# Optimization experiments

Hardware: AMD Instinct MI355X
Metric: run time of the kernel (lower is better)

Reference implementation:

```python
import jax, jax.numpy as jnp
import numpy as np

S, D = 16384, 1024


def setup_inputs() -> dict:
    key = jax.random.key(0)
    ks = jax.random.split(key, 7)
    stdv = 1.0 / np.sqrt(D)
    u = lambda k, shape: jax.random.uniform(k, shape, jnp.float32, -stdv, stdv)
    return {
        "x": jax.random.normal(ks[0], (S, D), jnp.float32),
        "Wq": u(ks[1], (D, D)), "bq": u(ks[2], (D,)),
        "Wk": u(ks[3], (D, D)), "bk": u(ks[4], (D,)),
        "Wv": u(ks[5], (D, D)), "bv": u(ks[6], (D,)),
    }


def reference(x, Wq, bq, Wk, bk, Wv, bv):
    # torch.nn.Linear: y = x @ W^T + b
    q = x @ Wq.T + bq          # [S, D]
    k = x @ Wk.T + bk          # [S, D]
    v = x @ Wv.T + bv          # [S, D]
    d = x.shape[-1]
    # NOTE: faithful to source -- scores are over the FEATURE axis: [D, D]
    scores = jnp.einsum('sd,se->de', q, k) / jnp.sqrt(jnp.float32(d))
    attn = jax.nn.softmax(scores, axis=-1)   # [D, D]
    out = v @ attn                           # [S, D]
    return out, attn
```

## Files before the change

kernel.cpp:

```cpp
#include <hip/hip_runtime.h>
#include <hip/hip_bf16.h>
#include <stdint.h>


#define S_ 16384
#define D_ 1024

typedef _Float16 half8 __attribute__((ext_vector_type(8)));
typedef _Float16 half4 __attribute__((ext_vector_type(4)));
typedef float f32x4 __attribute__((ext_vector_type(4)));

__device__ __forceinline__ void gload_lds16(const _Float16* g, _Float16* l) {
    __builtin_amdgcn_global_load_lds(
        (const __attribute__((address_space(1))) void*)g,
        (__attribute__((address_space(3))) void*)l, 16, 0, 0);
}

#define VM8() do { asm volatile("s_waitcnt vmcnt(8)" ::: "memory"); __builtin_amdgcn_sched_barrier(0); } while (0)
#define VM0() do { asm volatile("s_waitcnt vmcnt(0)" ::: "memory"); __builtin_amdgcn_sched_barrier(0); } while (0)
#define BAR() __builtin_amdgcn_s_barrier()
#define LGKM0() do { asm volatile("s_waitcnt lgkmcnt(0)" ::: "memory"); __builtin_amdgcn_sched_barrier(0); } while (0)
#define LGKM8() do { asm volatile("s_waitcnt lgkmcnt(8)" ::: "memory"); __builtin_amdgcn_sched_barrier(0); } while (0)
#define PRIO1() __builtin_amdgcn_s_setprio(1)
#define PRIO0() __builtin_amdgcn_s_setprio(0)

#define STAGEA(H, KT, NX) do { \
    const _Float16* _s = srcA + (size_t)((H) * 128) * lda + (size_t)(KT) * 64; \
    _Float16* _d = AsS + (NX) * 16384 + ((H) * 128 + 8 * w) * 64; \
    gload_lds16(_s, _d); \
    gload_lds16(_s + (size_t)64 * lda, _d + 4096); \
} while (0)

#define STAGEB(H, KT, NX) do { \
    const _Float16* _s = srcB + (size_t)((H) * 128) * ldb + (size_t)(KT) * 64; \
    _Float16* _d = BsS + (NX) * 16384 + ((H) * 128 + 8 * w) * 64; \
    gload_lds16(_s, _d); \
    gload_lds16(_s + (size_t)64 * ldb, _d + 4096); \
} while (0)

#define READA(PA, QA) do { _Pragma("unroll") \
    for (int fm = 0; fm < 4; ++fm) { \
        af[fm][0] = *(const half8*)((PA) + (((QA) * 128 + fm * 16) << 7) + cx0); \
        af[fm][1] = *(const half8*)((PA) + (((QA) * 128 + fm * 16) << 7) + cx1); } \
} while (0)

#define READB(PB, BF, QB) do { _Pragma("unroll") \
    for (int fn = 0; fn < 2; ++fn) { \
        BF[fn][0] = *(const half8*)((PB) + (((QB) * 128 + fn * 16) << 7) + cx0); \
        BF[fn][1] = *(const half8*)((PB) + (((QB) * 128 + fn * 16) << 7) + cx1); } \
} while (0)

#define MFMAB(QA, QB, BF) do { _Pragma("unroll") \
    for (int fm = 0; fm < 4; ++fm) { _Pragma("unroll") \
        for (int fn = 0; fn < 2; ++fn) { \
            f32x4 _c = acc[(QA) * 4 + fm][(QB) * 2 + fn]; \
            _c = __builtin_amdgcn_mfma_f32_16x16x32_f16(af[fm][0], BF[fn][0], _c, 0, 0, 0); \
            _c = __builtin_amdgcn_mfma_f32_16x16x32_f16(af[fm][1], BF[fn][1], _c, 0, 0, 0); \
            acc[(QA) * 4 + fm][(QB) * 2 + fn] = _c; } } \
} while (0)

__global__ __launch_bounds__(512, 2)
void gemm256(const _Float16* __restrict__ A, const _Float16* __restrict__ B,
             _Float16* __restrict__ C,
             int lda, int ldb, int ldc, int ksub, long long mn,
             int ntx, int ntxy, int cpx) {
    __shared__ _Float16 As[2][16384];
    __shared__ _Float16 Bs[2][16384];
    const int t = threadIdx.x;
    const int l = t & 63;
    const int w = t >> 6;
    const int wm = w >> 2, wn = w & 3;

    const int hb = blockIdx.x;
    const int lg = (hb & 7) * cpx + (hb >> 3);
    const int bz = lg / ntxy;
    const int rem = lg - bz * ntxy;
    const int by = rem / ntx;
    const int bx = rem - by * ntx;
    const size_t m0 = (size_t)by * 256;
    const size_t n0 = (size_t)bx * 256;
    const size_t k0 = (size_t)bz * (size_t)ksub;
    const long long coff = (long long)bz * mn;

    const int colsw = 8 * ((l & 7) ^ (l >> 3));
    const _Float16* srcA = A + (m0 + 8 * w + (l >> 3)) * (size_t)lda + k0 + colsw;
    const _Float16* srcB = B + (n0 + 8 * w + (l >> 3)) * (size_t)ldb + k0 + colsw;
    _Float16* AsS = &As[0][0];
    _Float16* BsS = &Bs[0][0];

    const int cx0 = (((l >> 4) << 4)) ^ ((l & 7) << 4);
    const int cx1 = (64 + ((l >> 4) << 4)) ^ ((l & 7) << 4);
    const char* basePA = (const char*)AsS + ((wm * 64 + (l & 15)) << 7);
    const char* basePB = (const char*)BsS + ((wn * 32 + (l & 15)) << 7);

    f32x4 acc[8][4] = {};
    half8 af[4][2], bf0[2][2], bf1[2][2];

    const int nk = ksub >> 6;

    STAGEA(0, 0, 0); STAGEB(0, 0, 0); STAGEB(1, 0, 0); STAGEA(1, 0, 0);
    STAGEA(0, 1, 1); STAGEB(0, 1, 1); STAGEB(1, 1, 1); STAGEA(1, 1, 1);

    for (int kt = 0; kt < nk; ++kt) {
        const int p = kt & 1;
        const int ks = kt + 2;
        const bool hs = ks < nk;
        const char* pA = basePA + p * 32768;
        const char* pB = basePB + p * 32768;

        if (kt == nk - 1) VM0(); else VM8();
        BAR();

        READA(pA, 0); READB(pB, bf0, 0);
        LGKM8();
        BAR(); LGKM0();
        PRIO1(); MFMAB(0, 0, bf0); PRIO0(); BAR();

        READB(pB, bf1, 1);
        if (hs) { STAGEA(0, ks, p); STAGEB(0, ks, p); }
        BAR(); LGKM0();
        PRIO1(); MFMAB(0, 1, bf1); PRIO0(); BAR();

        READA(pA, 1);
        if (hs) STAGEB(1, ks, p);
        BAR(); LGKM0();
        PRIO1(); MFMAB(1, 1, bf1); PRIO0(); BAR();

        if (hs) STAGEA(1, ks, p);
        PRIO1(); MFMAB(1, 0, bf0); PRIO0(); BAR();
    }

    char* lmy = (char*)AsS + w * 16384;
    const int cr = (l >> 4) << 2;
    const int cc = l & 15;
    _Float16* lw = (_Float16*)lmy;
#pragma unroll
    for (int h = 0; h < 2; ++h) {
#pragma unroll
        for (int mm = 0; mm < 4; ++mm) {
#pragma unroll
            for (int n = 0; n < 4; ++n) {
                const int lcol = (n >> 1) * 32 + (n & 1) * 16 + cc;
                const int lrow = mm * 16 + cr;
#pragma unroll
                for (int r = 0; r < 4; ++r)
                    lw[(lrow + r) * 68 + lcol] = (_Float16)acc[4 * h + mm][n][r];
            }
        }
        LGKM0();
        const size_t grow0 = m0 + (size_t)h * 128 + wm * 64;
#pragma unroll
        for (int i = 0; i < 32; ++i) {
            const int lrow = i * 2 + (l >> 5);
            const int lcol2 = (l & 31) * 2;
            const uint32_t v = *(const uint32_t*)(lw + lrow * 68 + lcol2);
            const int qb = lcol2 >> 5;
            const size_t col = n0 + qb * 128 + wn * 32 + (lcol2 & 31);
            __builtin_nontemporal_store(v,
                (uint32_t*)(C + coff + (long long)(grow0 + lrow) * ldc + col));
        }
        LGKM0();
    }
}

#define STG128(SRC, LD, DST, KT) do { \
    const _Float16* _s = (SRC) + (size_t)(KT) * 64; \
    _Float16* _d = (DST) + 8 * w * 64; \
    gload_lds16(_s, _d); \
    gload_lds16(_s + (size_t)32 * (LD), _d + 2048); \
    gload_lds16(_s + (size_t)64 * (LD), _d + 4096); \
    gload_lds16(_s + (size_t)96 * (LD), _d + 6144); \
} while (0)

__global__ __launch_bounds__(256, 2)
void gemm128(const _Float16* __restrict__ A, const _Float16* __restrict__ B,
             float* __restrict__ C, const float* __restrict__ bias,
             int lda, int ldb, int ldc, int ksub,
             int ntx, int cpx) {
    __shared__ _Float16 SM[32768];
    const int t = threadIdx.x;
    const int l = t & 63;
    const int w = t >> 6;
    const int wm = w >> 1, wn = w & 1;

    const int hb = blockIdx.x;
    const int lg = (hb & 7) * cpx + (hb >> 3);
    const int by = lg / ntx;
    const int bx = lg - by * ntx;
    const size_t m0 = (size_t)by * 128;
    const size_t n0 = (size_t)bx * 128;

    const int colsw = 8 * ((l & 7) ^ (l >> 3));
    const _Float16* srcA = A + (m0 + 8 * w + (l >> 3)) * (size_t)lda + colsw;
    const _Float16* srcB = B + (n0 + 8 * w + (l >> 3)) * (size_t)ldb + colsw;

    const int cx0 = (((l >> 4) << 4)) ^ ((l & 7) << 4);
    const int cx1 = (64 + ((l >> 4) << 4)) ^ ((l & 7) << 4);
    const char* basePA = (const char*)SM + ((wm * 64 + (l & 15)) << 7);
    const char* basePB = (const char*)SM + 32768 + ((wn * 64 + (l & 15)) << 7);

    f32x4 acc[4][4] = {};
    half8 af[4][2], bf[4][2];

    const int nk = ksub >> 6;

    STG128(srcA, lda, SM + 0, 0);        STG128(srcB, ldb, SM + 16384, 0);
    STG128(srcA, lda, SM + 8192, 1);     STG128(srcB, ldb, SM + 24576, 1);

    for (int kt = 0; kt < nk; ++kt) {
        const int p = kt & 1;
        const int ks = kt + 2;
        const bool hs = ks < nk;
        const char* pA = basePA + p * 16384;
        const char* pB = basePB + p * 16384;

        if (kt == nk - 1) VM0(); else VM8();
        BAR();

#pragma unroll
        for (int fm = 0; fm < 4; ++fm) {
            af[fm][0] = *(const half8*)(pA + ((fm * 16) << 7) + cx0);
            af[fm][1] = *(const half8*)(pA + ((fm * 16) << 7) + cx1);
        }
#pragma unroll
        for (int fn = 0; fn < 4; ++fn) {
            bf[fn][0] = *(const half8*)(pB + ((fn * 16) << 7) + cx0);
            bf[fn][1] = *(const half8*)(pB + ((fn * 16) << 7) + cx1);
        }
        LGKM0();
        PRIO1();
#pragma unroll
        for (int fm = 0; fm < 4; ++fm)
#pragma unroll
            for (int fn = 0; fn < 4; ++fn)
                acc[fm][fn] = __builtin_amdgcn_mfma_f32_16x16x32_f16(af[fm][0], bf[fn][0], acc[fm][fn], 0, 0, 0);
        PRIO0();
        BAR();

        if (hs) {
            STG128(srcA, lda, SM + p * 8192, ks);
            STG128(srcB, ldb, SM + 16384 + p * 8192, ks);
        }
        PRIO1();
#pragma unroll
        for (int fm = 0; fm < 4; ++fm)
#pragma unroll
            for (int fn = 0; fn < 4; ++fn)
                acc[fm][fn] = __builtin_amdgcn_mfma_f32_16x16x32_f16(af[fm][1], bf[fn][1], acc[fm][fn], 0, 0, 0);
        PRIO0();
        BAR();
    }

    float* lw = (float*)((char*)SM + w * 16384);
    const int cr = (l >> 4) << 2;
    const int cc = l & 15;
    float bb4[4];
#pragma unroll
    for (int fn = 0; fn < 4; ++fn)
        bb4[fn] = bias[n0 + wn * 64 + fn * 16 + cc];
#pragma unroll
    for (int h = 0; h < 2; ++h) {
#pragma unroll
        for (int mm2 = 0; mm2 < 2; ++mm2) {
            const int mm = h * 2 + mm2;
#pragma unroll
            for (int fn = 0; fn < 4; ++fn) {
                const int lcol = fn * 16 + cc;
                const int lrow = mm2 * 16 + cr;
#pragma unroll
                for (int r = 0; r < 4; ++r)
                    lw[(lrow + r) * 68 + lcol] = acc[mm][fn][r] + bb4[fn];
            }
        }
        LGKM0();
        const size_t grow0 = m0 + (size_t)wm * 64 + h * 32;
#pragma unroll
        for (int i = 0; i < 8; ++i) {
            const int lrow = i * 4 + (l >> 4);
            const int lcol = (l & 15) * 4;
            const f32x4 v = *(const f32x4*)(lw + lrow * 68 + lcol);
            __builtin_nontemporal_store(v,
                (f32x4*)(C + (size_t)(grow0 + lrow) * ldc + n0 + wn * 64 + lcol));
        }
        LGKM0();
    }
}

__global__ __launch_bounds__(256, 2)
void gemm_abt(const _Float16* __restrict__ A, const _Float16* __restrict__ B,
              float* __restrict__ C, int lda, int ldb, int ldc, int ksub,
              long long mn) {
    const int t = threadIdx.x;
    const int lane = t & 63;
    const int wave = t >> 6;
    const int wr = (wave >> 1) * 64;
    const int wc = (wave & 1) * 64;
    const size_t m0 = (size_t)blockIdx.y * 128;
    const size_t n0 = (size_t)blockIdx.x * 128;
    const size_t k0 = (size_t)blockIdx.z * (size_t)ksub;
    const long long coff = (long long)blockIdx.z * mn;

    __shared__ _Float16 As[128 * 32];
    __shared__ _Float16 Bs[128 * 32];

    f32x4 acc[4][4] = {};

    const _Float16* a0 = A + (m0 + (size_t)(t >> 2)) * (size_t)lda + k0 + (t & 3) * 8;
    const _Float16* a1 = a0 + (size_t)64 * lda;
    const _Float16* b0 = B + (n0 + (size_t)(t >> 2)) * (size_t)ldb + k0 + (t & 3) * 8;
    const _Float16* b1 = b0 + (size_t)64 * ldb;
    _Float16* AsW0 = As + wave * 512;
    _Float16* AsW1 = As + 2048 + wave * 512;
    _Float16* BsW0 = Bs + wave * 512;
    _Float16* BsW1 = Bs + 2048 + wave * 512;

    const int nk = ksub >> 5;
    for (int kt = 0; kt < nk; ++kt) {
        __syncthreads();
        gload_lds16(a0, AsW0);
        gload_lds16(a1, AsW1);
        gload_lds16(b0, BsW0);
        gload_lds16(b1, BsW1);
        a0 += 32; a1 += 32; b0 += 32; b1 += 32;
        __syncthreads();

        half8 af[4], bf[4];
#pragma unroll
        for (int i = 0; i < 4; ++i)
            af[i] = *(const half8*)(As + (wr + i * 16 + (lane & 15)) * 32 + (lane >> 4) * 8);
#pragma unroll
        for (int i = 0; i < 4; ++i)
            bf[i] = *(const half8*)(Bs + (wc + i * 16 + (lane & 15)) * 32 + (lane >> 4) * 8);
#pragma unroll
        for (int i = 0; i < 4; ++i)
#pragma unroll
            for (int j = 0; j < 4; ++j)
                acc[i][j] = __builtin_amdgcn_mfma_f32_16x16x32_f16(af[i], bf[j], acc[i][j], 0, 0, 0);
    }

    const int cr = (lane >> 4) * 4;
    const int cc = lane & 15;
#pragma unroll
    for (int i = 0; i < 4; ++i) {
#pragma unroll
        for (int j = 0; j < 4; ++j) {
            const size_t row0 = m0 + wr + i * 16 + cr;
            const size_t col = n0 + wc + j * 16 + cc;
#pragma unroll
            for (int r = 0; r < 4; ++r)
                C[coff + (long long)(row0 + r) * ldc + col] = acc[i][j][r];
        }
    }
}

template <int WRITE_ROW, int COLSUM>
__global__ __launch_bounds__(256)
void cast_transpose(const float* __restrict__ in, _Float16* __restrict__ outRow,
                    _Float16* __restrict__ outT, float* __restrict__ msum, int ldT) {
    __shared__ _Float16 tile[64][66];
    __shared__ float red[16][16][4];
    const int t = threadIdx.x;
    const int c0 = blockIdx.x * 64;
    const int r0 = blockIdx.y * 64;
    const int cg = t & 15;
    const int rb = t >> 4;
    f32x4 csum = {};
#pragma unroll
    for (int it = 0; it < 4; ++it) {
        const int rr = rb + it * 16;
        f32x4 v = *(const f32x4*)(in + (size_t)(r0 + rr) * 1024 + c0 + cg * 4);
        if (COLSUM) { csum[0] += v[0]; csum[1] += v[1]; csum[2] += v[2]; csum[3] += v[3]; }
        _Float16 h0 = (_Float16)v[0], h1 = (_Float16)v[1];
        _Float16 h2 = (_Float16)v[2], h3 = (_Float16)v[3];
        tile[rr][cg * 4 + 0] = h0; tile[rr][cg * 4 + 1] = h1;
        tile[rr][cg * 4 + 2] = h2; tile[rr][cg * 4 + 3] = h3;
        if (WRITE_ROW) {
            half4 h = {h0, h1, h2, h3};
            *(half4*)(outRow + (size_t)(r0 + rr) * 1024 + c0 + cg * 4) = h;
        }
    }
    if (COLSUM) {
        red[rb][cg][0] = csum[0]; red[rb][cg][1] = csum[1];
        red[rb][cg][2] = csum[2]; red[rb][cg][3] = csum[3];
    }
    __syncthreads();
    if (COLSUM && t < 64) {
        float s = 0.f;
#pragma unroll
        for (int k = 0; k < 16; ++k) s += red[k][t >> 2][t & 3];
        atomicAdd(msum + c0 + t, s);
    }
    const int i = t >> 2, ch = (t & 3) * 16;
    half8 h0v, h1v;
#pragma unroll
    for (int j = 0; j < 8; ++j) h0v[j] = tile[ch + j][i];
#pragma unroll
    for (int j = 0; j < 8; ++j) h1v[j] = tile[ch + 8 + j][i];
    *(half8*)(outT + (size_t)(c0 + i) * ldT + r0 + ch) = h0v;
    *(half8*)(outT + (size_t)(c0 + i) * ldT + r0 + ch + 8) = h1v;
}

__global__ __launch_bounds__(256)
void prep_w(const float* __restrict__ Wq, const float* __restrict__ Wk,
            const float* __restrict__ Wv, const float* __restrict__ bq,
            const float* __restrict__ m,
            _Float16* __restrict__ wq16, _Float16* __restrict__ wk16,
            _Float16* __restrict__ wvT16,
            float* __restrict__ u2, float* __restrict__ w) {
    __shared__ _Float16 tile[64][66];
    __shared__ float wred[4];
    const int b = blockIdx.x;
    const int t = threadIdx.x;

    if (b < 1024) {
        const bool isQ = b < 512;
        const int bb = isQ ? b : b - 512;
        const float* W = isQ ? Wq : Wk;
        _Float16* o = isQ ? wq16 : wk16;
        const size_t base = (size_t)bb * 2048 + (size_t)t * 8;
        const f32x4* p = (const f32x4*)(W + base);
        f32x4 x0 = p[0], x1 = p[1];
        half8 h;
        h[0] = (_Float16)x0[0]; h[1] = (_Float16)x0[1];
        h[2] = (_Float16)x0[2]; h[3] = (_Float16)x0[3];
        h[4] = (_Float16)x1[0]; h[5] = (_Float16)x1[1];
        h[6] = (_Float16)x1[2]; h[7] = (_Float16)x1[3];
        ((half8*)o)[bb * 256 + t] = h;
        const int col = (t * 8) & 1023;
        f32x4 m0 = *(const f32x4*)(m + col);
        f32x4 m1 = *(const f32x4*)(m + col + 4);
        float s = x0[0] * m0[0] + x0[1] * m0[1] + x0[2] * m0[2] + x0[3] * m0[3]
                + x1[0] * m1[0] + x1[1] * m1[1] + x1[2] * m1[2] + x1[3] * m1[3];
        for (int o2 = 32; o2; o2 >>= 1) s += __shfl_xor(s, o2);
        if ((t & 63) == 0) wred[t >> 6] = s;
        __syncthreads();
        if (t == 0) {
            const int rA = 2 * bb, rB = 2 * bb + 1;
            const float vA = wred[0] + wred[1];
            const float vB = wred[2] + wred[3];
            if (isQ) {
                u2[rA] = vA + 16384.0f * bq[rA];
                u2[rB] = vB + 16384.0f * bq[rB];
            } else {
                w[rA] = vA;
                w[rB] = vB;
            }
        }
        return;
    }

    const int bb = b - 1024;
    const int c0 = (bb & 15) * 64;
    const int r0 = (bb >> 4) * 64;
    const int cg = t & 15;
    const int rb = t >> 4;
#pragma unroll
    for (int it = 0; it < 4; ++it) {
        const int rr = rb + it * 16;
        f32x4 v = *(const f32x4*)(Wv + (size_t)(r0 + rr) * 1024 + c0 + cg * 4);
        tile[rr][cg * 4 + 0] = (_Float16)v[0];
        tile[rr][cg * 4 + 1] = (_Float16)v[1];
        tile[rr][cg * 4 + 2] = (_Float16)v[2];
        tile[rr][cg * 4 + 3] = (_Float16)v[3];
    }
    __syncthreads();
    const int i = t >> 2, ch = (t & 3) * 16;
    half8 h0v, h1v;
#pragma unroll
    for (int j = 0; j < 8; ++j) h0v[j] = tile[ch + j][i];
#pragma unroll
    for (int j = 0; j < 8; ++j) h1v[j] = tile[ch + 8 + j][i];
    *(half8*)(wvT16 + (size_t)(c0 + i) * 1024 + r0 + ch) = h0v;
    *(half8*)(wvT16 + (size_t)(c0 + i) * 1024 + r0 + ch + 8) = h1v;
}

__global__ void zero_vec(float* __restrict__ p, int n) {
    int i = blockIdx.x * 256 + threadIdx.x;
    if (i < n) p[i] = 0.f;
}

__global__ __launch_bounds__(256)
void reduce_g(const _Float16* __restrict__ part, _Float16* __restrict__ G16) {
    const size_t off = ((size_t)blockIdx.x * 256 + threadIdx.x) * 8;
    float s[8] = {};
    for (int z = 0; z < 16; ++z) {
        half8 v = *(const half8*)(part + (size_t)z * 1048576 + off);
#pragma unroll
        for (int j = 0; j < 8; ++j) s[j] += (float)v[j];
    }
    half8 o;
#pragma unroll
    for (int j = 0; j < 8; ++j) o[j] = (_Float16)s[j];
    *(half8*)(G16 + off) = o;
}

__global__ __launch_bounds__(256)
void reduce_cast(const float* __restrict__ part, _Float16* __restrict__ outh,
                 int nz, float scale) {
    const int idx = (blockIdx.x * 256 + threadIdx.x) * 4;
    f32x4 s = {};
    for (int z = 0; z < nz; ++z) {
        f32x4 v = *(const f32x4*)(part + (size_t)z * 1048576 + idx);
        s[0] += v[0]; s[1] += v[1]; s[2] += v[2]; s[3] += v[3];
    }
    half4 h;
    h[0] = (_Float16)(s[0] * scale); h[1] = (_Float16)(s[1] * scale);
    h[2] = (_Float16)(s[2] * scale); h[3] = (_Float16)(s[3] * scale);
    *(half4*)(outh + idx) = h;
}

__global__ __launch_bounds__(256)
void softmax_rows(const float* __restrict__ part, const float* __restrict__ u2,
                  const float* __restrict__ bq, const float* __restrict__ bk,
                  const float* __restrict__ w,
                  float* __restrict__ P, _Float16* __restrict__ PT) {
    const int a = blockIdx.x;
    const int t = threadIdx.x;
    __shared__ float red[8];
    const size_t off = (size_t)a * 1024 + t * 4;
    f32x4 s = {};
#pragma unroll
    for (int z = 0; z < 4; ++z) {
        f32x4 v = *(const f32x4*)(part + (size_t)z * 1048576 + off);
        s[0] += v[0]; s[1] += v[1]; s[2] += v[2]; s[3] += v[3];
    }
    const float ru = u2[a], rb = bq[a];
    f32x4 bk4 = *(const f32x4*)(bk + t * 4);
    f32x4 w4 = *(const f32x4*)(w + t * 4);
#pragma unroll
    for (int j = 0; j < 4; ++j) s[j] = (s[j] + ru * bk4[j] + rb * w4[j]) * 0.03125f;

    float m = fmaxf(fmaxf(s[0], s[1]), fmaxf(s[2], s[3]));
    for (int o = 32; o; o >>= 1) m = fmaxf(m, __shfl_xor(m, o));
    if ((t & 63) == 0) red[t >> 6] = m;
    __syncthreads();
    m = fmaxf(fmaxf(red[0], red[1]), fmaxf(red[2], red[3]));

    float e0 = expf(s[0] - m), e1 = expf(s[1] - m);
    float e2 = expf(s[2] - m), e3 = expf(s[3] - m);
    float sum = e0 + e1 + e2 + e3;
    for (int o = 32; o; o >>= 1) sum += __shfl_xor(sum, o);
    if ((t & 63) == 0) red[4 + (t >> 6)] = sum;
    __syncthreads();
    sum = red[4] + red[5] + red[6] + red[7];
    const float inv = 1.0f / sum;

    f32x4 o4 = {e0 * inv, e1 * inv, e2 * inv, e3 * inv};
    *(f32x4*)(P + off) = o4;
    const int b = t * 4;
    PT[(size_t)(b + 0) * 1024 + a] = (_Float16)o4[0];
    PT[(size_t)(b + 1) * 1024 + a] = (_Float16)o4[1];
    PT[(size_t)(b + 2) * 1024 + a] = (_Float16)o4[2];
    PT[(size_t)(b + 3) * 1024 + a] = (_Float16)o4[3];
}

__global__ __launch_bounds__(256)
void attn_bv(const float* __restrict__ attn, const float* __restrict__ bv,
             float* __restrict__ c) {
    const int j = blockIdx.x * 256 + threadIdx.x;
    const int a0 = blockIdx.y * 64;
    float s = 0.f;
#pragma unroll 4
    for (int k = 0; k < 64; ++k) {
        const int a = a0 + k;
        s += attn[(size_t)a * 1024 + j] * bv[a];
    }
    atomicAdd(c + j, s);
}

extern "C" void kernel_launch(void* const* d_in, const int* in_sizes, int n_in,
                              void* d_out, int out_size, void* d_ws, size_t ws_size,
                              hipStream_t stream) {
    const float* x  = (const float*)d_in[0];
    const float* Wq = (const float*)d_in[1];
    const float* bq = (const float*)d_in[2];
    const float* Wk = (const float*)d_in[3];
    const float* bk = (const float*)d_in[4];
    const float* Wv = (const float*)d_in[5];
    const float* bv = (const float*)d_in[6];
    float* out  = (float*)d_out;
    float* attn = out + (size_t)S_ * D_;

    char* ws = (char*)d_ws;
    float*    part  = (float*)ws;
    _Float16* partH = (_Float16*)ws;
    _Float16* x16   = (_Float16*)(ws + 33554432);
    _Float16* xT16  = (_Float16*)(ws + 67108864);
    _Float16* wq16  = (_Float16*)(ws + 100663296);
    _Float16* wk16  = (_Float16*)(ws + 102760448);
    _Float16* wvT16 = (_Float16*)(ws + 104857600);
    _Float16* G16   = (_Float16*)(ws + 106954752);
    _Float16* U16   = (_Float16*)(ws + 109051904);
    _Float16* PT    = (_Float16*)(ws + 111149056);
    _Float16* MT16  = (_Float16*)(ws + 113246208);
    float*    mvec  = (float*)(ws + 115343360);
    float*    u2    = mvec + 1024;
    float*    wv    = u2 + 1024;
    float*    cvec  = wv + 1024;

    zero_vec<<<16, 256, 0, stream>>>(mvec, 4096);
    cast_transpose<1, 1><<<dim3(16, 256), 256, 0, stream>>>(x, x16, xT16, mvec, S_);
    prep_w<<<1280, 256, 0, stream>>>(Wq, Wk, Wv, bq, mvec,
                                     wq16, wk16, wvT16, u2, wv);

    gemm256<<<256, 512, 0, stream>>>(xT16, xT16, partH,
                                     16384, 16384, 1024, 1024, 1048576LL,
                                     4, 16, 32);
    reduce_g<<<512, 256, 0, stream>>>(partH, G16);
    gemm_abt<<<dim3(8, 8, 4), 256, 0, stream>>>(wq16, G16, part,
                                                1024, 1024, 1024, 256, 1048576);
    reduce_cast<<<1024, 256, 0, stream>>>(part, U16, 4, 1.0f);
    gemm_abt<<<dim3(8, 8, 4), 256, 0, stream>>>(U16, wk16, part,
                                                1024, 1024, 1024, 256, 1048576);
    softmax_rows<<<1024, 256, 0, stream>>>(part, u2, bq, bk, wv, attn, PT);
    attn_bv<<<dim3(4, 16), 256, 0, stream>>>(attn, bv, cvec);
    gemm_abt<<<dim3(8, 8, 4), 256, 0, stream>>>(PT, wvT16, part,
                                                1024, 1024, 1024, 256, 1048576);
    reduce_cast<<<1024, 256, 0, stream>>>(part, MT16, 4, 1.0f);
    gemm128<<<1024, 256, 0, stream>>>(x16, MT16, out, cvec,
                                      1024, 1024, 1024, 1024, 8, 128);
}
```

Measured before the change: 185.1 us.

## Replace output GEMM with 128x512-tile kernel and widen gemm256 epilogue stores

The final x·M GEMM now runs as a new 512-thread kernel with a 128x512 output tile and a K-step of 32. Each block reuses its A tile across four times more columns, and the grid shrinks from 1024 blocks to 256. Separately, the gemm256 epilogue now stages the full 128x256 half tile in shared memory behind block barriers, so each lane can write 16-byte rows instead of 4-byte pieces. The risks are more shared memory and registers per block, lower occupancy, more barriers per K step, and only 256 blocks to fill the GPU.

```diff
diff --git a/kernel.cpp b/kernel.cpp
--- a/kernel.cpp
+++ b/kernel.cpp
@@ -17,6 +17,7 @@
 }
 
 #define VM8() do { asm volatile("s_waitcnt vmcnt(8)" ::: "memory"); __builtin_amdgcn_sched_barrier(0); } while (0)
+#define VM5() do { asm volatile("s_waitcnt vmcnt(5)" ::: "memory"); __builtin_amdgcn_sched_barrier(0); } while (0)
 #define VM0() do { asm volatile("s_waitcnt vmcnt(0)" ::: "memory"); __builtin_amdgcn_sched_barrier(0); } while (0)
 #define BAR() __builtin_amdgcn_s_barrier()
 #define LGKM0() do { asm volatile("s_waitcnt lgkmcnt(0)" ::: "memory"); __builtin_amdgcn_sched_barrier(0); } while (0)
@@ -64,8 +65,9 @@
              _Float16* __restrict__ C,
              int lda, int ldb, int ldc, int ksub, long long mn,
              int ntx, int ntxy, int cpx) {
-    __shared__ _Float16 As[2][16384];
-    __shared__ _Float16 Bs[2][16384];
+    __shared__ _Float16 SM2[65536];
+    _Float16* AsS = SM2;
+    _Float16* BsS = SM2 + 32768;
     const int t = threadIdx.x;
     const int l = t & 63;
     const int w = t >> 6;
@@ -85,8 +87,6 @@
     const int colsw = 8 * ((l & 7) ^ (l >> 3));
     const _Float16* srcA = A + (m0 + 8 * w + (l >> 3)) * (size_t)lda + k0 + colsw;
     const _Float16* srcB = B + (n0 + 8 * w + (l >> 3)) * (size_t)ldb + k0 + colsw;
-    _Float16* AsS = &As[0][0];
-    _Float16* BsS = &Bs[0][0];
 
     const int cx0 = (((l >> 4) << 4)) ^ ((l & 7) << 4);
     const int cx1 = (64 + ((l >> 4) << 4)) ^ ((l & 7) << 4);
@@ -130,157 +130,144 @@
         PRIO1(); MFMAB(1, 0, bf0); PRIO0(); BAR();
     }
 
-    char* lmy = (char*)AsS + w * 16384;
+    _Float16* eb = SM2;
     const int cr = (l >> 4) << 2;
     const int cc = l & 15;
-    _Float16* lw = (_Float16*)lmy;
 #pragma unroll
     for (int h = 0; h < 2; ++h) {
+        BAR();
 #pragma unroll
         for (int mm = 0; mm < 4; ++mm) {
 #pragma unroll
             for (int n = 0; n < 4; ++n) {
-                const int lcol = (n >> 1) * 32 + (n & 1) * 16 + cc;
-                const int lrow = mm * 16 + cr;
+                const int lrow0 = wm * 64 + mm * 16 + cr;
+                const int lcol = (n >> 1) * 128 + wn * 32 + (n & 1) * 16 + cc;
 #pragma unroll
                 for (int r = 0; r < 4; ++r)
-                    lw[(lrow + r) * 68 + lcol] = (_Float16)acc[4 * h + mm][n][r];
+                    eb[(lrow0 + r) * 264 + lcol] = (_Float16)acc[h * 4 + mm][n][r];
             }
         }
         LGKM0();
-        const size_t grow0 = m0 + (size_t)h * 128 + wm * 64;
-#pragma unroll
-        for (int i = 0; i < 32; ++i) {
-            const int lrow = i * 2 + (l >> 5);
-            const int lcol2 = (l & 31) * 2;
-            const uint32_t v = *(const uint32_t*)(lw + lrow * 68 + lcol2);
-            const int qb = lcol2 >> 5;
-            const size_t col = n0 + qb * 128 + wn * 32 + (lcol2 & 31);
+        BAR();
+#pragma unroll
+        for (int i = 0; i < 8; ++i) {
+            const int lrow = w * 16 + i * 2 + (l >> 5);
+            const half8 v = *(const half8*)(eb + lrow * 264 + (l & 31) * 8);
+            const size_t row = m0 + (size_t)h * 128 + lrow;
+            const size_t col = n0 + (l & 31) * 8;
             __builtin_nontemporal_store(v,
-                (uint32_t*)(C + coff + (long long)(grow0 + lrow) * ldc + col));
+                (half8*)(C + coff + (long long)row * ldc + col));
         }
         LGKM0();
     }
 }
 
-#define STG128(SRC, LD, DST, KT) do { \
-    const _Float16* _s = (SRC) + (size_t)(KT) * 64; \
-    _Float16* _d = (DST) + 8 * w * 64; \
-    gload_lds16(_s, _d); \
-    gload_lds16(_s + (size_t)32 * (LD), _d + 2048); \
-    gload_lds16(_s + (size_t)64 * (LD), _d + 4096); \
-    gload_lds16(_s + (size_t)96 * (LD), _d + 6144); \
+#define STGO(KT, NX) do { \
+    const _Float16* _sa = srcA + (size_t)(KT) * 32; \
+    gload_lds16(_sa, AsS + (NX) * 4096 + w * 512); \
+    const _Float16* _sb = srcB + (size_t)(KT) * 32; \
+    _Float16* _db = BsS + (NX) * 16384 + w * 2048; \
+    gload_lds16(_sb, _db); \
+    gload_lds16(_sb + 16 * 1024, _db + 512); \
+    gload_lds16(_sb + 32 * 1024, _db + 1024); \
+    gload_lds16(_sb + 48 * 1024, _db + 1536); \
 } while (0)
 
-__global__ __launch_bounds__(256, 2)
-void gemm128(const _Float16* __restrict__ A, const _Float16* __restrict__ B,
-             float* __restrict__ C, const float* __restrict__ bias,
-             int lda, int ldb, int ldc, int ksub,
-             int ntx, int cpx) {
-    __shared__ _Float16 SM[32768];
+__global__ __launch_bounds__(512, 2)
+void gemm_out(const _Float16* __restrict__ A, const _Float16* __restrict__ B,
+              float* __restrict__ C, const float* __restrict__ bias) {
+    __shared__ _Float16 SM[40960];
+    _Float16* AsS = SM;
+    _Float16* BsS = SM + 8192;
     const int t = threadIdx.x;
     const int l = t & 63;
     const int w = t >> 6;
-    const int wm = w >> 1, wn = w & 1;
+    const int wm = w >> 2, wn = w & 3;
 
     const int hb = blockIdx.x;
-    const int lg = (hb & 7) * cpx + (hb >> 3);
-    const int by = lg / ntx;
-    const int bx = lg - by * ntx;
+    const int lg = (hb & 7) * 32 + (hb >> 3);
+    const int by = lg >> 1;
+    const int bx = lg & 1;
     const size_t m0 = (size_t)by * 128;
-    const size_t n0 = (size_t)bx * 128;
-
-    const int colsw = 8 * ((l & 7) ^ (l >> 3));
-    const _Float16* srcA = A + (m0 + 8 * w + (l >> 3)) * (size_t)lda + colsw;
-    const _Float16* srcB = B + (n0 + 8 * w + (l >> 3)) * (size_t)ldb + colsw;
-
-    const int cx0 = (((l >> 4) << 4)) ^ ((l & 7) << 4);
-    const int cx1 = (64 + ((l >> 4) << 4)) ^ ((l & 7) << 4);
-    const char* basePA = (const char*)SM + ((wm * 64 + (l & 15)) << 7);
-    const char* basePB = (const char*)SM + 32768 + ((wn * 64 + (l & 15)) << 7);
-
-    f32x4 acc[4][4] = {};
-    half8 af[4][2], bf[4][2];
-
-    const int nk = ksub >> 6;
-
-    STG128(srcA, lda, SM + 0, 0);        STG128(srcB, ldb, SM + 16384, 0);
-    STG128(srcA, lda, SM + 8192, 1);     STG128(srcB, ldb, SM + 24576, 1);
+    const size_t n0 = (size_t)bx * 512;
+
+    const int colsw = 8 * ((l & 3) ^ ((l >> 2) & 3));
+    const _Float16* srcA = A + (m0 + w * 16 + (l >> 2)) * (size_t)1024 + colsw;
+    const _Float16* srcB = B + (n0 + w * 64 + (l >> 2)) * (size_t)1024 + colsw;
+
+    const int cx = (((l >> 4) ^ (l & 3)) << 4);
+    const char* basePA = (const char*)AsS + ((wm * 64 + (l & 15)) << 6) + cx;
+    const char* basePB = (const char*)BsS + ((wn * 128 + (l & 15)) << 6) + cx;
+
+    f32x4 acc[4][8] = {};
+    half8 af[4], bf[8];
+
+    const int nk = 32;
+
+    STGO(0, 0);
+    STGO(1, 1);
 
     for (int kt = 0; kt < nk; ++kt) {
         const int p = kt & 1;
         const int ks = kt + 2;
         const bool hs = ks < nk;
-        const char* pA = basePA + p * 16384;
-        const char* pB = basePB + p * 16384;
-
-        if (kt == nk - 1) VM0(); else VM8();
+        const char* pA = basePA + p * 8192;
+        const char* pB = basePB + p * 32768;
+
+        if (kt == nk - 1) VM0(); else VM5();
         BAR();
 
 #pragma unroll
-        for (int fm = 0; fm < 4; ++fm) {
-            af[fm][0] = *(const half8*)(pA + ((fm * 16) << 7) + cx0);
-            af[fm][1] = *(const half8*)(pA + ((fm * 16) << 7) + cx1);
-        }
-#pragma unroll
-        for (int fn = 0; fn < 4; ++fn) {
-            bf[fn][0] = *(const half8*)(pB + ((fn * 16) << 7) + cx0);
-            bf[fn][1] = *(const half8*)(pB + ((fn * 16) << 7) + cx1);
+        for (int fm = 0; fm < 4; ++fm)
+            af[fm] = *(const half8*)(pA + fm * 1024);
+#pragma unroll
+        for (int fn = 0; fn < 8; ++fn)
+            bf[fn] = *(const half8*)(pB + fn * 1024);
+        LGKM0();
+        PRIO1();
+#pragma unroll
+        for (int fm = 0; fm < 4; ++fm)
+#pragma unroll
+            for (int fn = 0; fn < 4; ++fn)
+                acc[fm][fn] = __builtin_amdgcn_mfma_f32_16x16x32_f16(af[fm], bf[fn], acc[fm][fn], 0, 0, 0);
+        PRIO0();
+        BAR();
+
+        if (hs) STGO(ks, p);
+        PRIO1();
+#pragma unroll
+        for (int fm = 0; fm < 4; ++fm)
+#pragma unroll
+            for (int fn = 4; fn < 8; ++fn)
+                acc[fm][fn] = __builtin_amdgcn_mfma_f32_16x16x32_f16(af[fm], bf[fn], acc[fm][fn], 0, 0, 0);
+        PRIO0();
+        BAR();
+    }
+
+    float* lw = (float*)SM + w * 2112;
+    const int cr = (l >> 4) << 2;
+    const int cc = l & 15;
+    float bb[8];
+#pragma unroll
+    for (int fn = 0; fn < 8; ++fn)
+        bb[fn] = bias[n0 + wn * 128 + fn * 16 + cc];
+#pragma unroll
+    for (int mm = 0; mm < 4; ++mm) {
+#pragma unroll
+        for (int fn = 0; fn < 8; ++fn) {
+            const int lcol = fn * 16 + cc;
+#pragma unroll
+            for (int r = 0; r < 4; ++r)
+                lw[(cr + r) * 132 + lcol] = acc[mm][fn][r] + bb[fn];
         }
         LGKM0();
-        PRIO1();
-#pragma unroll
-        for (int fm = 0; fm < 4; ++fm)
-#pragma unroll
-            for (int fn = 0; fn < 4; ++fn)
-                acc[fm][fn] = __builtin_amdgcn_mfma_f32_16x16x32_f16(af[fm][0], bf[fn][0], acc[fm][fn], 0, 0, 0);
-        PRIO0();
-        BAR();
-
-        if (hs) {
-            STG128(srcA, lda, SM + p * 8192, ks);
-            STG128(srcB, ldb, SM + 16384 + p * 8192, ks);
-        }
-        PRIO1();
-#pragma unroll
-        for (int fm = 0; fm < 4; ++fm)
-#pragma unroll
-            for (int fn = 0; fn < 4; ++fn)
-                acc[fm][fn] = __builtin_amdgcn_mfma_f32_16x16x32_f16(af[fm][1], bf[fn][1], acc[fm][fn], 0, 0, 0);
-        PRIO0();
-        BAR();
-    }
-
-    float* lw = (float*)((char*)SM + w * 16384);
-    const int cr = (l >> 4) << 2;
-    const int cc = l & 15;
-    float bb4[4];
-#pragma unroll
-    for (int fn = 0; fn < 4; ++fn)
-        bb4[fn] = bias[n0 + wn * 64 + fn * 16 + cc];
-#pragma unroll
-    for (int h = 0; h < 2; ++h) {
-#pragma unroll
-        for (int mm2 = 0; mm2 < 2; ++mm2) {
-            const int mm = h * 2 + mm2;
-#pragma unroll
-            for (int fn = 0; fn < 4; ++fn) {
-                const int lcol = fn * 16 + cc;
-                const int lrow = mm2 * 16 + cr;
-#pragma unroll
-                for (int r = 0; r < 4; ++r)
-                    lw[(lrow + r) * 68 + lcol] = acc[mm][fn][r] + bb4[fn];
-            }
-        }
-        LGKM0();
-        const size_t grow0 = m0 + (size_t)wm * 64 + h * 32;
 #pragma unroll
         for (int i = 0; i < 8; ++i) {
-            const int lrow = i * 4 + (l >> 4);
-            const int lcol = (l & 15) * 4;
-            const f32x4 v = *(const f32x4*)(lw + lrow * 68 + lcol);
-            __builtin_nontemporal_store(v,
-                (f32x4*)(C + (size_t)(grow0 + lrow) * ldc + n0 + wn * 64 + lcol));
+            const int lrow = i * 2 + (l >> 5);
+            const f32x4 v = *(const f32x4*)(lw + lrow * 132 + (l & 31) * 4);
+            const size_t row = m0 + wm * 64 + mm * 16 + lrow;
+            const size_t col = n0 + wn * 128 + (l & 31) * 4;
+            __builtin_nontemporal_store(v, (f32x4*)(C + row * 1024 + col));
         }
         LGKM0();
     }
@@ -617,6 +604,5 @@
     gemm_abt<<<dim3(8, 8, 4), 256, 0, stream>>>(PT, wvT16, part,
                                                 1024, 1024, 1024, 256, 1048576);
     reduce_cast<<<1024, 256, 0, stream>>>(part, MT16, 4, 1.0f);
-    gemm128<<<1024, 256, 0, stream>>>(x16, MT16, out, cvec,
-                                      1024, 1024, 1024, 1024, 8, 128);
-}
+    gemm_out<<<256, 512, 0, stream>>>(x16, MT16, out, cvec);
+}
```

Result: no change. 187.5 us (+1.3%).
